# Kernel optimization log

Measured on AMD Instinct MI355X. Metric: run time of the kernel, lower is better.

Reference implementation:

```python
import jax, jax.numpy as jnp
import numpy as np

# (in_ch, out_ch) per conv layer per SA stage (use_xyz adds +3 to first in-ch)
DIMS = {1: [(3, 64), (64, 64), (64, 128)],
        2: [(131, 128), (128, 128), (128, 256)],
        3: [(259, 256), (256, 512), (512, 1024)]}
B, N = 32, 4096


def setup_inputs() -> dict:
    key = jax.random.key(0)
    key, k = jax.random.split(key)
    inp = {"pointcloud": jax.random.uniform(k, (B, N, 3), jnp.float32)}
    for s in (1, 2, 3):
        for l, (ci, co) in enumerate(DIMS[s]):
            key, k1, k2, k3 = jax.random.split(key, 4)
            inp[f"w{s}{l}"] = jax.random.normal(k1, (ci, co), jnp.float32) * (1.0 / np.sqrt(ci))
            # eval-mode BatchNorm folded to per-channel scale g and bias b
            inp[f"g{s}{l}"] = 1.0 + 0.1 * jax.random.normal(k2, (co,), jnp.float32)
            inp[f"b{s}{l}"] = 0.1 * jax.random.normal(k3, (co,), jnp.float32)
    return inp


def fps(xyz, npoint):
    """Farthest point sampling. xyz: (B,N,3) -> idx (B,npoint) int32. First index is 0."""
    n = xyz.shape[1]
    def one(pts):
        def body(carry, _):
            dist, last = carry
            d = jnp.sum((pts - pts[last]) ** 2, axis=-1)
            dist = jnp.minimum(dist, d)
            nxt = jnp.argmax(dist).astype(jnp.int32)
            return (dist, nxt), nxt
        init = (jnp.full((n,), 1e10, pts.dtype), jnp.int32(0))
        _, idxs = jax.lax.scan(body, init, None, length=npoint - 1)
        return jnp.concatenate([jnp.zeros((1,), jnp.int32), idxs])
    return jax.vmap(one)(xyz)


def ball_query(xyz, centers, radius, nsample):
    """xyz (B,N,3), centers (B,S,3) -> idx (B,S,nsample): first nsample in-ball point
    indices, deficits padded with the first found index (matches CUDA ball_query)."""
    n = xyz.shape[1]
    d2 = jnp.sum((centers[:, :, None, :] - xyz[:, None, :, :]) ** 2, axis=-1)  # (B,S,N)
    keyv = jnp.where(d2 < radius * radius, jnp.arange(n)[None, None, :], n)
    sk = jnp.sort(keyv, axis=-1)[..., :nsample]  # ascending valid indices, pad = n
    first = sk[..., :1]
    idx = jnp.where(sk == n, first, sk)
    return jnp.clip(idx, 0, n - 1)


def gather(pts, idx):
    """pts (B,N,C), idx (B,...) -> (B,...,C)"""
    return jax.vmap(lambda p, i: p[i])(pts, idx)


def shared_mlp(x, params):
    """x (..., Cin); each layer: 1x1 conv (matmul) + folded-BN affine + ReLU."""
    for w, g, b in params:
        x = jax.nn.relu(jnp.einsum('...c,cd->...d', x, w) * g + b)
    return x


def sa_module(xyz, feat, npoint, radius, nsample, params):
    ctr_idx = fps(xyz, npoint)
    new_xyz = gather(xyz, ctr_idx)                        # (B,S,3)
    idx = ball_query(xyz, new_xyz, radius, nsample)       # (B,S,K)
    g_xyz = gather(xyz, idx) - new_xyz[:, :, None, :]     # (B,S,K,3) centered
    grouped = g_xyz if feat is None else jnp.concatenate([g_xyz, gather(feat, idx)], axis=-1)
    h = shared_mlp(grouped, params)                       # (B,S,K,Cout)
    return new_xyz, jnp.max(h, axis=2)                    # max-pool over neighbors


def reference(pointcloud, w10, g10, b10, w11, g11, b11, w12, g12, b12,
              w20, g20, b20, w21, g21, b21, w22, g22, b22,
              w30, g30, b30, w31, g31, b31, w32, g32, b32):
    p1 = [(w10, g10, b10), (w11, g11, b11), (w12, g12, b12)]
    p2 = [(w20, g20, b20), (w21, g21, b21), (w22, g22, b22)]
    p3 = [(w30, g30, b30), (w31, g31, b31), (w32, g32, b32)]
    xyz = pointcloud[..., :3]
    xyz, feat = sa_module(xyz, None, 512, 0.2, 64, p1)
    xyz, feat = sa_module(xyz, feat, 128, 0.4, 64, p2)
    # group-all SA: one group containing all points, xyz NOT centered
    grouped = jnp.concatenate([xyz, feat], axis=-1)[:, None]  # (B,1,S,259)
    h = shared_mlp(grouped, p3)                                # (B,1,S,1024)
    return jnp.max(h, axis=2)[:, 0]                            # (B,1024)
```

## Files before the change

kernel.cpp:

```cpp
#include <hip/hip_runtime.h>
#include <math.h>

#define NTH 256

using short8 = __attribute__((ext_vector_type(8))) short;
using f32x4  = __attribute__((ext_vector_type(4))) float;

__device__ __forceinline__ unsigned short f2bf(float x) {
    unsigned u = __float_as_uint(x);
    u += 0x7fff + ((u >> 16) & 1);
    return (unsigned short)(u >> 16);
}
__device__ __forceinline__ float bf2f(unsigned short h) {
    return __uint_as_float(((unsigned)h) << 16);
}

template<int CTRL>
__device__ __forceinline__ unsigned long long dppmax(unsigned long long k) {
    unsigned lo = (unsigned)k, hi = (unsigned)(k >> 32);
    unsigned plo = (unsigned)__builtin_amdgcn_update_dpp(0, (int)lo, CTRL, 0xF, 0xF, true);
    unsigned phi = (unsigned)__builtin_amdgcn_update_dpp(0, (int)hi, CTRL, 0xF, 0xF, true);
    unsigned long long p = ((unsigned long long)phi << 32) | plo;
    return p > k ? p : k;
}

template<int N, int NPOINT, int NTHR, int NPC, bool INIT, bool SPILL>
__device__ __forceinline__ void fps_body(
    const float* __restrict__ xyz, float* __restrict__ out_xyz, int b, int it0,
    float* __restrict__ pts , float* __restrict__ ctr ,
    unsigned long long* __restrict__ wkey ,
    float* __restrict__ sdist, int* __restrict__ slast)
{
    constexpr int PT = N / NTHR;
    constexpr int NW = NTHR / 64;
    const int tid  = threadIdx.x;
    const int lane = tid & 63;
    const int w    = tid >> 6;
    const float* src = xyz + (size_t)b * N * 3;

    __builtin_amdgcn_s_setprio(1);

    for (int e = tid; e < N * 3; e += NTHR) pts[e] = src[e];

    float px[PT], py[PT], pz[PT], dist[PT];
    unsigned klo[PT];
#pragma unroll
    for (int j = 0; j < PT; ++j) {
        int i = j * NTHR + tid;
        px[j] = src[i * 3 + 0]; py[j] = src[i * 3 + 1]; pz[j] = src[i * 3 + 2];
        klo[j] = ~(unsigned)i;
        dist[j] = 1e10f;
    }
    int last = 0;
    if constexpr (!INIT) {
        const float* sd = sdist + (size_t)b * N;
#pragma unroll
        for (int j = 0; j < PT; ++j) dist[j] = sd[j * NTHR + tid];
        last = slast[b];
    } else {
        if (tid == 0) { ctr[0] = src[0]; ctr[1] = src[1]; ctr[2] = src[2]; }
    }
    __syncthreads();

    constexpr int CBEG = INIT ? 1 : 0;
    for (int c = CBEG; c < NPC; ++c) {
        const float lx = pts[last * 3 + 0];
        const float ly = pts[last * 3 + 1];
        const float lz = pts[last * 3 + 2];
        unsigned long long best = 0ull;
#pragma unroll
        for (int j = 0; j < PT; ++j) {
            float dx = px[j] - lx, dy = py[j] - ly, dz = pz[j] - lz;
            float d = __fadd_rn(__fadd_rn(__fmul_rn(dx, dx), __fmul_rn(dy, dy)),
                                __fmul_rn(dz, dz));
            float nd = fminf(dist[j], d);
            dist[j] = nd;
            unsigned long long key =
                ((unsigned long long)__float_as_uint(nd) << 32) | (unsigned long long)klo[j];
            best = (key > best) ? key : best;
        }
        best = dppmax<0xB1>(best);
        best = dppmax<0x4E>(best);
        best = dppmax<0x141>(best);
        best = dppmax<0x140>(best);
        best = dppmax<0x142>(best);
        best = dppmax<0x143>(best);
        const int p = (c & 1) * NW;
        if (lane == 63) wkey[p + w] = best;
        __syncthreads();
        unsigned long long K0[NW];
#pragma unroll
        for (int v = 0; v < NW; ++v) K0[v] = wkey[p + v];
#pragma unroll
        for (int st = NW / 2; st > 0; st >>= 1)
#pragma unroll
            for (int v = 0; v < st; ++v) K0[v] = (K0[v + st] > K0[v]) ? K0[v + st] : K0[v];
        last = (int)(~(unsigned)K0[0]);
        if (tid == 0) {
            ctr[c * 3 + 0] = pts[last * 3 + 0];
            ctr[c * 3 + 1] = pts[last * 3 + 1];
            ctr[c * 3 + 2] = pts[last * 3 + 2];
        }
    }
    __syncthreads();
    if constexpr (SPILL) {
        float* sd = sdist + (size_t)b * N;
#pragma unroll
        for (int j = 0; j < PT; ++j) sd[j * NTHR + tid] = dist[j];
        if (tid == 0) slast[b] = last;
    }
    float* dst = out_xyz + ((size_t)b * NPOINT + (it0 - CBEG)) * 3;
    for (int e = tid; e < NPC * 3; e += NTHR) dst[e] = ctr[e];
    __builtin_amdgcn_s_setprio(0);
}

template<int N, int NPOINT>
__device__ __forceinline__ void fps2_wave_body(
    const float* __restrict__ xyz, float* __restrict__ out_xyz, int b,
    float* __restrict__ pts , float* __restrict__ ctr )
{
    const int tid = threadIdx.x;
    const float* src = xyz + (size_t)b * N * 3;
    for (int e = tid; e < N * 3; e += NTH) pts[e] = src[e];
    __syncthreads();
    if (tid < 64) {
        __builtin_amdgcn_s_setprio(1);
        constexpr int PT = N / 64;
        const int lane = tid;
        float px[PT], py[PT], pz[PT], dist[PT];
        unsigned klo[PT];
#pragma unroll
        for (int j = 0; j < PT; ++j) {
            int i = j * 64 + lane;
            px[j] = pts[i * 3 + 0]; py[j] = pts[i * 3 + 1]; pz[j] = pts[i * 3 + 2];
            dist[j] = 1e10f;
            klo[j] = ~(unsigned)i;
        }
        int last = 0;
        if (lane == 0) { ctr[0] = pts[0]; ctr[1] = pts[1]; ctr[2] = pts[2]; }
        for (int it = 1; it < NPOINT; ++it) {
            const float lx = pts[last * 3 + 0];
            const float ly = pts[last * 3 + 1];
            const float lz = pts[last * 3 + 2];
            unsigned long long best = 0ull;
#pragma unroll
            for (int j = 0; j < PT; ++j) {
                float dx = px[j] - lx, dy = py[j] - ly, dz = pz[j] - lz;
                float d = __fadd_rn(__fadd_rn(__fmul_rn(dx, dx), __fmul_rn(dy, dy)),
                                    __fmul_rn(dz, dz));
                float nd = fminf(dist[j], d);
                dist[j] = nd;
                unsigned long long key =
                    ((unsigned long long)__float_as_uint(nd) << 32) | (unsigned long long)klo[j];
                best = (key > best) ? key : best;
            }
            best = dppmax<0xB1>(best);
            best = dppmax<0x4E>(best);
            best = dppmax<0x141>(best);
            best = dppmax<0x140>(best);
            best = dppmax<0x142>(best);
            best = dppmax<0x143>(best);
            unsigned long long g = __shfl(best, 63);
            last = (int)(~(unsigned)g);
            if (lane == 0) {
                ctr[it * 3 + 0] = pts[last * 3 + 0];
                ctr[it * 3 + 1] = pts[last * 3 + 1];
                ctr[it * 3 + 2] = pts[last * 3 + 2];
            }
        }
        __builtin_amdgcn_s_setprio(0);
    }
    __syncthreads();
    float* dst = out_xyz + (size_t)b * NPOINT * 3;
    for (int e = tid; e < NPOINT * 3; e += NTH) dst[e] = ctr[e];
}

#define PREP_TOT 813056
__device__ __forceinline__ void prep_body(
    int gid, int stride,
    const float* __restrict__ w0, const float* __restrict__ w1, const float* __restrict__ w2,
    const float* __restrict__ w3, const float* __restrict__ w4, const float* __restrict__ w5,
    const float* __restrict__ w6, const float* __restrict__ w7, const float* __restrict__ w8,
    unsigned short* __restrict__ outw)
{
    const int K_[9]    = {3, 64, 64, 131, 128, 128, 259, 256, 512};
    const int N_[9]    = {64, 64, 128, 128, 128, 256, 256, 512, 1024};
    const int E_[9]    = {2048, 4096, 8192, 20480, 16384, 32768, 73728, 131072, 524288};
    const int base_[9] = {0, 4096, 12288, 28672, 69632, 102400, 167936, 315392, 577536};
    const int PCF_[9]  = {0, 0, 0, 128, 0, 0, 256, 0, 0};
    const float* W_[9] = {w0, w1, w2, w3, w4, w5, w6, w7, w8};
    for (; gid < PREP_TOT; gid += stride) {
        int i = 0, t = gid;
        while (t >= E_[i]) { t -= E_[i]; ++i; }
        const int Nn = N_[i];
        const int k8 = t / (Nn * 8);
        const int rem = t - k8 * Nn * 8;
        const int col = rem >> 3, j = rem & 7;
        const int k = k8 * 8 + j;
        float v = 0.f;
        if (k < K_[i]) {
            int ks = k;
            const int pcf = PCF_[i];
            if (pcf > 0) ks = (k < pcf) ? (k + 3) : (k - pcf);
            v = W_[i][(size_t)ks * Nn + col];
        }
        unsigned short hi = f2bf(v);
        unsigned short lo = f2bf(v - bf2f(hi));
        outw[base_[i] + t] = hi;
        outw[base_[i] + E_[i] + t] = lo;
    }
}

template<int K, int NSUB, int NOFF, int NFULL, int RTILES, int SX, int SY, bool FINAL>
__device__ __forceinline__ void mfma_layer(
    const unsigned short* __restrict__ whi, const unsigned short* __restrict__ wlo,
    const float* __restrict__ gm, const float* __restrict__ bt,
    const unsigned short* __restrict__ Xhi, const unsigned short* __restrict__ Xlo,
    unsigned short* __restrict__ Yhi, unsigned short* __restrict__ Ylo,
    float* outp, int tid)
{
    constexpr int KP  = (K + 31) & ~31;
    constexpr int KC  = KP / 32;
    constexpr int NTW = NSUB / 64;
    static_assert(NSUB % 64 == 0, "col split");
    const int w = tid >> 6, lane = tid & 63;
    const int lr = lane & 15, lg = lane >> 4;
    const int colbase = NOFF + w * (NSUB / 4);

    f32x4 acc[RTILES][NTW];
#pragma unroll
    for (int m = 0; m < RTILES; ++m)
#pragma unroll
        for (int t = 0; t < NTW; ++t) acc[m][t] = f32x4{0.f, 0.f, 0.f, 0.f};

    const unsigned short* xh0 = Xhi + lr * SX + lg * 8;
    const unsigned short* xl0 = Xlo + lr * SX + lg * 8;

    for (int kc = 0; kc < KC; ++kc) {
        const size_t krow = (size_t)(kc * 4 + lg) * NFULL * 8;
        short8 bh[NTW], bl[NTW];
#pragma unroll
        for (int t = 0; t < NTW; ++t) {
            const int col = colbase + t * 16 + lr;
            bh[t] = *reinterpret_cast<const short8*>(whi + krow + (size_t)col * 8);
            bl[t] = *reinterpret_cast<const short8*>(wlo + krow + (size_t)col * 8);
        }
#pragma unroll
        for (int m = 0; m < RTILES; ++m) {
            short8 ah = *reinterpret_cast<const short8*>(xh0 + m * 16 * SX + kc * 32);
            short8 al = *reinterpret_cast<const short8*>(xl0 + m * 16 * SX + kc * 32);
#pragma unroll
            for (int t = 0; t < NTW; ++t) {
                acc[m][t] = __builtin_amdgcn_mfma_f32_16x16x32_bf16(ah, bh[t], acc[m][t], 0, 0, 0);
                acc[m][t] = __builtin_amdgcn_mfma_f32_16x16x32_bf16(ah, bl[t], acc[m][t], 0, 0, 0);
                acc[m][t] = __builtin_amdgcn_mfma_f32_16x16x32_bf16(al, bh[t], acc[m][t], 0, 0, 0);
            }
        }
    }
#pragma unroll
    for (int t = 0; t < NTW; ++t) {
        const int col = colbase + t * 16 + lr;
        const float gv = gm[col], bv = bt[col];
        if constexpr (FINAL) {
            float mx = 0.f;
#pragma unroll
            for (int m = 0; m < RTILES; ++m)
#pragma unroll
                for (int r = 0; r < 4; ++r)
                    mx = fmaxf(mx, fmaxf(fmaf(acc[m][t][r], gv, bv), 0.f));
            mx = fmaxf(mx, __shfl_xor(mx, 16));
            mx = fmaxf(mx, __shfl_xor(mx, 32));
            if (lg == 0)
                atomicMax(reinterpret_cast<int*>(outp) + col, __float_as_int(mx));
        } else {
#pragma unroll
            for (int m = 0; m < RTILES; ++m)
#pragma unroll
                for (int r = 0; r < 4; ++r) {
                    float v = fmaxf(fmaf(acc[m][t][r], gv, bv), 0.f);
                    unsigned short hi = f2bf(v);
                    unsigned short lo = f2bf(v - bf2f(hi));
                    const int row = m * 16 + lg * 4 + r;
                    Yhi[row * SY + col] = hi;
                    Ylo[row * SY + col] = lo;
                }
        }
    }
}

template<int CF, int C0, int C1, int C2, int R>
struct SaCfg {
    static constexpr int CIN = 3 + CF;
    static constexpr int KP0 = (CIN + 31) & ~31;
    static constexpr int SX = KP0 + 8, SY1 = C0 + 8, SY2 = C1 + 8;
    static constexpr int RT = R / 16;
    static constexpr int OFF_Y1 = 0;
    static constexpr int OFF_X = 2 * R * SY1;
    static constexpr int XSZ = 2 * R * SX, Y2SZ = 2 * R * SY2;
    static constexpr int TOT = OFF_X + (XSZ > Y2SZ ? XSZ : Y2SZ);
    static constexpr int BYTES = TOT * 2 + 264 * 4;
};

template<int CF, int C0, int C1, int C2, int R>
__device__ __forceinline__ void sa_body(
    unsigned short* __restrict__ sm, int* __restrict__ bqm,
    int b, int cs, int S, int half,
    const float* __restrict__ src_xyz, const float* __restrict__ src_feat,
    const float* __restrict__ centers,
    const unsigned short* __restrict__ w0h, const unsigned short* __restrict__ w0l,
    const unsigned short* __restrict__ w1h, const unsigned short* __restrict__ w1l,
    const unsigned short* __restrict__ w2h, const unsigned short* __restrict__ w2l,
    const float* __restrict__ g0, const float* __restrict__ b0,
    const float* __restrict__ g1, const float* __restrict__ b1,
    const float* __restrict__ g2, const float* __restrict__ b2,
    float* __restrict__ out_feat, int N, float r2)
{
    using C = SaCfg<CF, C0, C1, C2, R>;
    constexpr int TPR = NTH / R;
    const int tid  = threadIdx.x;
    const int lane = tid & 63;
    const int w    = tid >> 6;
    const int bs   = b * S + cs;

    const float cx = centers[(size_t)bs * 3 + 0];
    const float cy = centers[(size_t)bs * 3 + 1];
    const float cz = centers[(size_t)bs * 3 + 2];

    {
        const int seg = N >> 2;
        const float* px = src_xyz + (size_t)b * N * 3;
        int count = 0, first = -1;
        const int bend = (w + 1) * seg;
        for (int base = w * seg; base < bend && count < 64; base += 64) {
            int i = base + lane;
            float dx = px[i * 3 + 0] - cx, dy = px[i * 3 + 1] - cy, dz = px[i * 3 + 2] - cz;
            float d2 = __fadd_rn(__fadd_rn(__fmul_rn(dx, dx), __fmul_rn(dy, dy)),
                                 __fmul_rn(dz, dz));
            bool inb = d2 < r2;
            unsigned long long m = __ballot(inb);
            if (first < 0 && m) first = base + (__ffsll(m) - 1);
            if (inb) {
                int pos = count + (int)__popcll(m & ((1ull << lane) - 1ull));
                if (pos < 64) bqm[w * 64 + pos] = i;
            }
            count += (int)__popcll(m);
        }
        if (lane == 0) {
            bqm[256 + w] = count > 64 ? 64 : count;
            bqm[260 + w] = first;
        }
    }
    __syncthreads();

    unsigned short* Xhi = sm + C::OFF_X;    unsigned short* Xlo = Xhi + R * C::SX;
    unsigned short* Y1h = sm + C::OFF_Y1;   unsigned short* Y1l = Y1h + R * C::SY1;
    unsigned short* Y2h = sm + C::OFF_X;    unsigned short* Y2l = Y2h + R * C::SY2;

    {
        const int r = tid / TPR, s = tid % TPR;
        int pid;
        {
            const int cA = bqm[256 + 0], cB = bqm[256 + 1], cC = bqm[256 + 2], cD = bqm[256 + 3];
            const int tot = cA + cB + cC + cD;
            int t = half * R + r;
            if (t < tot) {
                int ww = 0;
                if (t >= cA) { t -= cA; ww = 1;
                    if (t >= cB) { t -= cB; ww = 2;
                        if (t >= cC) { t -= cC; ww = 3; } } }
                pid = bqm[ww * 64 + t];
            } else {
                const int fA = bqm[260 + 0], fB = bqm[260 + 1], fC = bqm[260 + 2], fD = bqm[260 + 3];
                pid = fA >= 0 ? fA : (fB >= 0 ? fB : (fC >= 0 ? fC : (fD >= 0 ? fD : (N - 1))));
            }
        }
        unsigned short* xh = Xhi + r * C::SX;
        unsigned short* xl = Xlo + r * C::SX;
        if constexpr (CF > 0) {
            constexpr int CPT = CF / TPR;
            const float* frow = src_feat + ((size_t)b * N + pid) * CF + s * CPT;
#pragma unroll
            for (int q = 0; q < CPT / 4; ++q) {
                float4 v4 = *reinterpret_cast<const float4*>(frow + q * 4);
                ushort4 h, l;
                h.x = f2bf(v4.x); l.x = f2bf(v4.x - bf2f(h.x));
                h.y = f2bf(v4.y); l.y = f2bf(v4.y - bf2f(h.y));
                h.z = f2bf(v4.z); l.z = f2bf(v4.z - bf2f(h.z));
                h.w = f2bf(v4.w); l.w = f2bf(v4.w - bf2f(h.w));
                *reinterpret_cast<ushort4*>(xh + s * CPT + q * 4) = h;
                *reinterpret_cast<ushort4*>(xl + s * CPT + q * 4) = l;
            }
        }
        if (s < 3) {
            float p = src_xyz[((size_t)b * N + pid) * 3 + s]
                      - (s == 0 ? cx : (s == 1 ? cy : cz));
            unsigned short hi = f2bf(p), lo = f2bf(p - bf2f(hi));
            xh[CF + s] = hi; xl[CF + s] = lo;
        }
        constexpr int PADPER = (C::KP0 - C::CIN + TPR - 1) / TPR;
#pragma unroll
        for (int q = 0; q < PADPER; ++q) {
            int c = C::CIN + s * PADPER + q;
            if (c < C::KP0) { xh[c] = 0; xl[c] = 0; }
        }
    }
    __syncthreads();
    mfma_layer<C::CIN, C0, 0, C0, C::RT, C::SX, C::SY1, false>(
        w0h, w0l, g0, b0, Xhi, Xlo, Y1h, Y1l, nullptr, tid);
    __syncthreads();
    mfma_layer<C0, C1, 0, C1, C::RT, C::SY1, C::SY2, false>(
        w1h, w1l, g1, b1, Y1h, Y1l, Y2h, Y2l, nullptr, tid);
    __syncthreads();
    mfma_layer<C1, C2, 0, C2, C::RT, C::SY2, 0, true>(
        w2h, w2l, g2, b2, Y2h, Y2l, nullptr, nullptr,
        out_feat + (size_t)bs * C2, tid);
}

template<int N1>
__global__ __launch_bounds__(NTH) void k_fps1a_prep(
    const float* __restrict__ pc, float* __restrict__ nxyz1,
    const float* __restrict__ w0, const float* __restrict__ w1, const float* __restrict__ w2,
    const float* __restrict__ w3, const float* __restrict__ w4, const float* __restrict__ w5,
    const float* __restrict__ w6, const float* __restrict__ w7, const float* __restrict__ w8,
    unsigned short* __restrict__ outw,
    float* __restrict__ sdist, int* __restrict__ slast,
    float4* __restrict__ z1, int n1, float4* __restrict__ z2, int n2,
    float4* __restrict__ z3, int n3, int nfps, int nprep)
{
    __shared__ float pts[N1 * 3];
    __shared__ float ctr[256 * 3];
    __shared__ unsigned long long wkey[2 * (NTH / 64)];
    if ((int)blockIdx.x < nfps) {
        fps_body<N1, 512, NTH, 256, true, true>(pc, nxyz1, blockIdx.x, 1,
                                                pts, ctr, wkey, sdist, slast);
    } else if ((int)blockIdx.x < nfps + nprep) {
        prep_body((blockIdx.x - nfps) * NTH + threadIdx.x, nprep * NTH,
                  w0, w1, w2, w3, w4, w5, w6, w7, w8, outw);
    } else {
        const int zid = (blockIdx.x - nfps - nprep) * NTH + threadIdx.x;
        const int zs  = (gridDim.x - nfps - nprep) * NTH;
        const float4 zv = make_float4(0.f, 0.f, 0.f, 0.f);
        for (int i = zid; i < n1; i += zs) z1[i] = zv;
        for (int i = zid; i < n2; i += zs) z2[i] = zv;
        for (int i = zid; i < n3; i += zs) z3[i] = zv;
    }
}

__global__ __launch_bounds__(NTH) void k_fps1b_sa1h1(
    const float* __restrict__ pc, float* __restrict__ nxyz1,
    float* __restrict__ sdist, int* __restrict__ slast,
    const unsigned short* __restrict__ w0h, const unsigned short* __restrict__ w0l,
    const unsigned short* __restrict__ w1h, const unsigned short* __restrict__ w1l,
    const unsigned short* __restrict__ w2h, const unsigned short* __restrict__ w2l,
    const float* __restrict__ g0, const float* __restrict__ b0,
    const float* __restrict__ g1, const float* __restrict__ b1,
    const float* __restrict__ g2, const float* __restrict__ b2,
    float* __restrict__ feat1, float r2)
{
    constexpr int FPSB = 4096 * 3 * 4 + 256 * 3 * 4 + 2 * (NTH / 64) * 8;
    constexpr int SAB  = SaCfg<0, 64, 64, 128, 64>::BYTES;
    constexpr int BYTES = FPSB > SAB ? FPSB : SAB;
    __shared__ __align__(16) char raw[BYTES];
    if ((int)blockIdx.x < 32) {
        float* pts = (float*)raw;
        float* ctr = (float*)(raw + 4096 * 3 * 4);
        unsigned long long* wkey = (unsigned long long*)(raw + 4096 * 3 * 4 + 256 * 3 * 4);
        fps_body<4096, 512, NTH, 256, false, false>(pc, nxyz1, blockIdx.x, 256,
                                                    pts, ctr, wkey, sdist, slast);
    } else {
        const int blk = blockIdx.x - 32;
        const int b = blk >> 8, cs = blk & 255;
        unsigned short* sm = (unsigned short*)raw;
        int* bqm = (int*)(raw + SaCfg<0, 64, 64, 128, 64>::TOT * 2);
        sa_body<0, 64, 64, 128, 64>(sm, bqm, b, cs, 512, 0,
                                    pc, nullptr, nxyz1,
                                    w0h, w0l, w1h, w1l, w2h, w2l,
                                    g0, b0, g1, b1, g2, b2, feat1, 4096, r2);
    }
}

__global__ __launch_bounds__(NTH) void k_fps2_sa1h2(
    const float* __restrict__ pc, const float* __restrict__ nxyz1,
    float* __restrict__ nxyz2,
    const unsigned short* __restrict__ w0h, const unsigned short* __restrict__ w0l,
    const unsigned short* __restrict__ w1h, const unsigned short* __restrict__ w1l,
    const unsigned short* __restrict__ w2h, const unsigned short* __restrict__ w2l,
    const float* __restrict__ g0, const float* __restrict__ b0,
    const float* __restrict__ g1, const float* __restrict__ b1,
    const float* __restrict__ g2, const float* __restrict__ b2,
    float* __restrict__ feat1, float r2)
{
    constexpr int FPSB = 512 * 3 * 4 + 128 * 3 * 4;
    constexpr int SAB  = SaCfg<0, 64, 64, 128, 64>::BYTES;
    constexpr int BYTES = FPSB > SAB ? FPSB : SAB;
    __shared__ __align__(16) char raw[BYTES];
    if ((int)blockIdx.x < 32) {
        float* pts = (float*)raw;
        float* ctr = (float*)(raw + 512 * 3 * 4);
        fps2_wave_body<512, 128>(nxyz1, nxyz2, blockIdx.x, pts, ctr);
    } else {
        const int blk = blockIdx.x - 32;
        const int b = blk >> 8, cs = 256 + (blk & 255);
        unsigned short* sm = (unsigned short*)raw;
        int* bqm = (int*)(raw + SaCfg<0, 64, 64, 128, 64>::TOT * 2);
        sa_body<0, 64, 64, 128, 64>(sm, bqm, b, cs, 512, 0,
                                    pc, nullptr, nxyz1,
                                    w0h, w0l, w1h, w1l, w2h, w2l,
                                    g0, b0, g1, b1, g2, b2, feat1, 4096, r2);
    }
}

__global__ __launch_bounds__(NTH) void k_sa2(
    const float* __restrict__ nxyz1, const float* __restrict__ feat1,
    const float* __restrict__ nxyz2,
    const unsigned short* __restrict__ w0h, const unsigned short* __restrict__ w0l,
    const unsigned short* __restrict__ w1h, const unsigned short* __restrict__ w1l,
    const unsigned short* __restrict__ w2h, const unsigned short* __restrict__ w2l,
    const float* __restrict__ g0, const float* __restrict__ b0,
    const float* __restrict__ g1, const float* __restrict__ b1,
    const float* __restrict__ g2, const float* __restrict__ b2,
    float* __restrict__ feat2, float r2)
{
    using C = SaCfg<128, 128, 128, 256, 32>;
    __shared__ __align__(16) char raw[C::BYTES];
    const int half = blockIdx.x & 1;
    const int cb   = blockIdx.x >> 1;
    const int b = cb >> 7, cs = cb & 127;
    unsigned short* sm = (unsigned short*)raw;
    int* bqm = (int*)(raw + C::TOT * 2);
    sa_body<128, 128, 128, 256, 32>(sm, bqm, b, cs, 128, half,
                                    nxyz1, feat1, nxyz2,
                                    w0h, w0l, w1h, w1l, w2h, w2l,
                                    g0, b0, g1, b1, g2, b2, feat2, 512, r2);
}

template<int CF, int C0, int C1, int C2>
__global__ __launch_bounds__(NTH) void head_mfma(
    const float* __restrict__ xyz, const float* __restrict__ feat,
    const unsigned short* __restrict__ w0h, const unsigned short* __restrict__ w0l,
    const unsigned short* __restrict__ w1h, const unsigned short* __restrict__ w1l,
    const unsigned short* __restrict__ w2h, const unsigned short* __restrict__ w2l,
    const float* __restrict__ g0, const float* __restrict__ b0,
    const float* __restrict__ g1, const float* __restrict__ b1,
    const float* __restrict__ g2, const float* __restrict__ b2,
    float* __restrict__ out, int Np)
{
    constexpr int R = 16;
    constexpr int CIN = 3 + CF;
    constexpr int KP0 = (CIN + 31) & ~31;
    constexpr int SX = KP0 + 8, SY1 = C0 + 8, SY2 = C1 + 8;
    constexpr int OFF_Y1 = 0;
    constexpr int OFF_X  = 2 * R * SY1;
    constexpr int XSZ = 2 * R * SX, Y2SZ = 2 * R * SY2;
    constexpr int TOT = OFF_X + (XSZ > Y2SZ ? XSZ : Y2SZ);
    __shared__ __align__(16) unsigned short sm[TOT];
    constexpr int TPR = NTH / R;

    const int tid = threadIdx.x;
    const int chunks = Np / R;
    const int b  = blockIdx.x / chunks;
    const int r0 = (blockIdx.x % chunks) * R;

    unsigned short* Xhi = sm + OFF_X;   unsigned short* Xlo = Xhi + R * SX;
    unsigned short* Y1h = sm + OFF_Y1;  unsigned short* Y1l = Y1h + R * SY1;
    unsigned short* Y2h = sm + OFF_X;   unsigned short* Y2l = Y2h + R * SY2;

    {
        const int r = tid / TPR, s = tid % TPR;
        const int row = r0 + r;
        unsigned short* xh = Xhi + r * SX;
        unsigned short* xl = Xlo + r * SX;
        constexpr int CPT = CF / TPR;
        const float* frow = feat + ((size_t)b * Np + row) * CF + s * CPT;
#pragma unroll
        for (int q = 0; q < CPT / 4; ++q) {
            float4 v4 = *reinterpret_cast<const float4*>(frow + q * 4);
            ushort4 h, l;
            h.x = f2bf(v4.x); l.x = f2bf(v4.x - bf2f(h.x));
            h.y = f2bf(v4.y); l.y = f2bf(v4.y - bf2f(h.y));
            h.z = f2bf(v4.z); l.z = f2bf(v4.z - bf2f(h.z));
            h.w = f2bf(v4.w); l.w = f2bf(v4.w - bf2f(h.w));
            *reinterpret_cast<ushort4*>(xh + s * CPT + q * 4) = h;
            *reinterpret_cast<ushort4*>(xl + s * CPT + q * 4) = l;
        }
        if (s < 3) {
            float p = xyz[((size_t)b * Np + row) * 3 + s];
            unsigned short hi = f2bf(p), lo = f2bf(p - bf2f(hi));
            xh[CF + s] = hi; xl[CF + s] = lo;
        }
        constexpr int PADPER = (KP0 - CIN + TPR - 1) / TPR;
#pragma unroll
        for (int q = 0; q < PADPER; ++q) {
            int c = CIN + s * PADPER + q;
            if (c < KP0) { xh[c] = 0; xl[c] = 0; }
        }
    }
    __syncthreads();
    mfma_layer<CIN, C0, 0, C0, 1, SX, SY1, false>(w0h, w0l, g0, b0, Xhi, Xlo, Y1h, Y1l, nullptr, tid);
    __syncthreads();
    mfma_layer<C0, C1, 0, C1, 1, SY1, SY2, false>(w1h, w1l, g1, b1, Y1h, Y1l, Y2h, Y2l, nullptr, tid);
    __syncthreads();
    float* op = out + (size_t)b * C2;
    mfma_layer<C1, C2 / 2, 0,      C2, 1, SY2, 0, true>(w2h, w2l, g2, b2, Y2h, Y2l, nullptr, nullptr, op, tid);
    mfma_layer<C1, C2 / 2, C2 / 2, C2, 1, SY2, 0, true>(w2h, w2l, g2, b2, Y2h, Y2l, nullptr, nullptr, op, tid);
}

extern "C" void kernel_launch(void* const* d_in, const int* in_sizes, int n_in,
                              void* d_out, int out_size, void* d_ws, size_t ws_size,
                              hipStream_t stream)
{
    (void)in_sizes; (void)n_in; (void)ws_size;
    const int B = 32;
    const float* pc = (const float*)d_in[0];
    const float* W[27];
    for (int i = 0; i < 27; ++i) W[i] = (const float*)d_in[1 + i];
    float* out = (float*)d_out;

    char* ws = (char*)d_ws;
    size_t off = 0;
    auto take = [&](size_t bytes) {
        void* p = ws + off;
        off += (bytes + 255) & ~(size_t)255;
        return p;
    };
    float* nxyz1 = (float*)take((size_t)B * 512 * 3 * 4);
    float* feat1 = (float*)take((size_t)B * 512 * 128 * 4);
    float* nxyz2 = (float*)take((size_t)B * 128 * 3 * 4);
    float* feat2 = (float*)take((size_t)B * 128 * 256 * 4);
    unsigned short* wf = (unsigned short*)take((size_t)1626112 * 2);
    float* sdist = (float*)take((size_t)B * 4096 * 4);
    int*   slast = (int*)take((size_t)B * 4);

    const int E_[9]    = {2048, 4096, 8192, 20480, 16384, 32768, 73728, 131072, 524288};
    const int base_[9] = {0, 4096, 12288, 28672, 69632, 102400, 167936, 315392, 577536};
    const unsigned short* wh[9]; const unsigned short* wl[9];
    for (int i = 0; i < 9; ++i) { wh[i] = wf + base_[i]; wl[i] = wf + base_[i] + E_[i]; }

    const float r2_1 = (float)(0.2 * 0.2);
    const float r2_2 = (float)(0.4 * 0.4);

    k_fps1a_prep<4096><<<32 + 512 + 64, NTH, 0, stream>>>(
        pc, nxyz1,
        W[0], W[3], W[6], W[9], W[12], W[15], W[18], W[21], W[24],
        wf, sdist, slast,
        (float4*)feat1, B * 512 * 128 / 4,
        (float4*)feat2, B * 128 * 256 / 4,
        (float4*)out,   out_size / 4,
        32, 512);

    k_fps1b_sa1h1<<<32 + B * 256, NTH, 0, stream>>>(
        pc, nxyz1, sdist, slast,
        wh[0], wl[0], wh[1], wl[1], wh[2], wl[2],
        W[1], W[2], W[4], W[5], W[7], W[8],
        feat1, r2_1);

    k_fps2_sa1h2<<<32 + B * 256, NTH, 0, stream>>>(
        pc, nxyz1, nxyz2,
        wh[0], wl[0], wh[1], wl[1], wh[2], wl[2],
        W[1], W[2], W[4], W[5], W[7], W[8],
        feat1, r2_1);

    k_sa2<<<B * 128 * 2, NTH, 0, stream>>>(
        nxyz1, feat1, nxyz2,
        wh[3], wl[3], wh[4], wl[4], wh[5], wl[5],
        W[10], W[11], W[13], W[14], W[16], W[17],
        feat2, r2_2);

    head_mfma<256, 256, 512, 1024><<<B * 8, NTH, 0, stream>>>(
        nxyz2, feat2,
        wh[6], wl[6], wh[7], wl[7], wh[8], wl[8],
        W[19], W[20], W[22], W[23], W[25], W[26],
        out, 128);
}
```

Measured before the change: 607.4 us.

## Merge FPS1b, FPS2 and SA1 into one kernel with per-chunk release/acquire flags

```diff
diff --git a/kernel.cpp b/kernel.cpp
--- a/kernel.cpp
+++ b/kernel.cpp
@@ -24,11 +24,11 @@
     return p > k ? p : k;
 }
 
-template<int N, int NPOINT, int NTHR, int NPC, bool INIT, bool SPILL>
-__device__ __forceinline__ void fps_body(
-    const float* __restrict__ xyz, float* __restrict__ out_xyz, int b, int it0,
-    float* __restrict__ pts , float* __restrict__ ctr ,
-    unsigned long long* __restrict__ wkey ,
+template<int N, int NPOINT, int NTHR, int NPC>
+__device__ __forceinline__ void fps1a_body(
+    const float* __restrict__ xyz, float* __restrict__ out_xyz, int b,
+    float* __restrict__ pts, float* __restrict__ ctr ,
+    unsigned long long* __restrict__ wkey,
     float* __restrict__ sdist, int* __restrict__ slast)
 {
     constexpr int PT = N / NTHR;
@@ -39,7 +39,6 @@
     const float* src = xyz + (size_t)b * N * 3;
 
     __builtin_amdgcn_s_setprio(1);
-
     for (int e = tid; e < N * 3; e += NTHR) pts[e] = src[e];
 
     float px[PT], py[PT], pz[PT], dist[PT];
@@ -52,18 +51,10 @@
         dist[j] = 1e10f;
     }
     int last = 0;
-    if constexpr (!INIT) {
-        const float* sd = sdist + (size_t)b * N;
-#pragma unroll
-        for (int j = 0; j < PT; ++j) dist[j] = sd[j * NTHR + tid];
-        last = slast[b];
-    } else {
-        if (tid == 0) { ctr[0] = src[0]; ctr[1] = src[1]; ctr[2] = src[2]; }
-    }
-    __syncthreads();
-
-    constexpr int CBEG = INIT ? 1 : 0;
-    for (int c = CBEG; c < NPC; ++c) {
+    if (tid == 0) { ctr[0] = src[0]; ctr[1] = src[1]; ctr[2] = src[2]; }
+    __syncthreads();
+
+    for (int c = 1; c < NPC; ++c) {
         const float lx = pts[last * 3 + 0];
         const float ly = pts[last * 3 + 1];
         const float lz = pts[last * 3 + 2];
@@ -103,21 +94,107 @@
         }
     }
     __syncthreads();
-    if constexpr (SPILL) {
+    {
         float* sd = sdist + (size_t)b * N;
 #pragma unroll
         for (int j = 0; j < PT; ++j) sd[j * NTHR + tid] = dist[j];
         if (tid == 0) slast[b] = last;
     }
-    float* dst = out_xyz + ((size_t)b * NPOINT + (it0 - CBEG)) * 3;
+    float* dst = out_xyz + (size_t)b * NPOINT * 3;
     for (int e = tid; e < NPC * 3; e += NTHR) dst[e] = ctr[e];
+    __builtin_amdgcn_s_setprio(0);
+}
+
+template<int N, int NTHR>
+__device__ __forceinline__ void fps1b_body(
+    const float* __restrict__ xyz, float* __restrict__ out_xyz , int b,
+    float* __restrict__ pts, float* __restrict__ ctr ,
+    unsigned long long* __restrict__ wkey,
+    const float* __restrict__ sdist, const int* __restrict__ slast,
+    int* __restrict__ flags)
+{
+    constexpr int PT = N / NTHR;
+    constexpr int NW = NTHR / 64;
+    const int tid  = threadIdx.x;
+    const int lane = tid & 63;
+    const int w    = tid >> 6;
+    const float* src = xyz + (size_t)b * N * 3;
+
+    __builtin_amdgcn_s_setprio(1);
+    for (int e = tid; e < N * 3; e += NTHR) pts[e] = src[e];
+
+    float px[PT], py[PT], pz[PT], dist[PT];
+    unsigned klo[PT];
+#pragma unroll
+    for (int j = 0; j < PT; ++j) {
+        int i = j * NTHR + tid;
+        px[j] = src[i * 3 + 0]; py[j] = src[i * 3 + 1]; pz[j] = src[i * 3 + 2];
+        klo[j] = ~(unsigned)i;
+    }
+    {
+        const float* sd = sdist + (size_t)b * N;
+#pragma unroll
+        for (int j = 0; j < PT; ++j) dist[j] = sd[j * NTHR + tid];
+    }
+    int last = slast[b];
+    __syncthreads();
+
+    for (int c = 0; c < 256; ++c) {
+        const float lx = pts[last * 3 + 0];
+        const float ly = pts[last * 3 + 1];
+        const float lz = pts[last * 3 + 2];
+        unsigned long long best = 0ull;
+#pragma unroll
+        for (int j = 0; j < PT; ++j) {
+            float dx = px[j] - lx, dy = py[j] - ly, dz = pz[j] - lz;
+            float d = __fadd_rn(__fadd_rn(__fmul_rn(dx, dx), __fmul_rn(dy, dy)),
+                                __fmul_rn(dz, dz));
+            float nd = fminf(dist[j], d);
+            dist[j] = nd;
+            unsigned long long key =
+                ((unsigned long long)__float_as_uint(nd) << 32) | (unsigned long long)klo[j];
+            best = (key > best) ? key : best;
+        }
+        best = dppmax<0xB1>(best);
+        best = dppmax<0x4E>(best);
+        best = dppmax<0x141>(best);
+        best = dppmax<0x140>(best);
+        best = dppmax<0x142>(best);
+        best = dppmax<0x143>(best);
+        const int p = (c & 1) * NW;
+        if (lane == 63) wkey[p + w] = best;
+        __syncthreads();
+        unsigned long long K0[NW];
+#pragma unroll
+        for (int v = 0; v < NW; ++v) K0[v] = wkey[p + v];
+#pragma unroll
+        for (int st = NW / 2; st > 0; st >>= 1)
+#pragma unroll
+            for (int v = 0; v < st; ++v) K0[v] = (K0[v + st] > K0[v]) ? K0[v + st] : K0[v];
+        last = (int)(~(unsigned)K0[0]);
+        if (tid == 0) {
+            ctr[c * 3 + 0] = pts[last * 3 + 0];
+            ctr[c * 3 + 1] = pts[last * 3 + 1];
+            ctr[c * 3 + 2] = pts[last * 3 + 2];
+        }
+        if ((c & 63) == 63) {
+            const int q = c >> 6;
+            __syncthreads();
+            float* dst = out_xyz + ((size_t)b * 512 + 256 + q * 64) * 3;
+            for (int e = tid; e < 192; e += NTHR) dst[e] = ctr[q * 192 + e];
+            __syncthreads();
+            if (tid == 0)
+                __hip_atomic_store(&flags[b * 4 + q], 1,
+                                   __ATOMIC_RELEASE, __HIP_MEMORY_SCOPE_AGENT);
+        }
+    }
     __builtin_amdgcn_s_setprio(0);
 }
 
 template<int N, int NPOINT>
 __device__ __forceinline__ void fps2_wave_body(
     const float* __restrict__ xyz, float* __restrict__ out_xyz, int b,
-    float* __restrict__ pts , float* __restrict__ ctr )
+    float* __restrict__ pts, float* __restrict__ ctr)
 {
     const int tid = threadIdx.x;
     const float* src = xyz + (size_t)b * N * 3;
@@ -425,14 +502,14 @@
     unsigned short* __restrict__ outw,
     float* __restrict__ sdist, int* __restrict__ slast,
     float4* __restrict__ z1, int n1, float4* __restrict__ z2, int n2,
-    float4* __restrict__ z3, int n3, int nfps, int nprep)
+    float4* __restrict__ z3, int n3, float4* __restrict__ z4, int n4,
+    int nfps, int nprep)
 {
     __shared__ float pts[N1 * 3];
     __shared__ float ctr[256 * 3];
     __shared__ unsigned long long wkey[2 * (NTH / 64)];
     if ((int)blockIdx.x < nfps) {
-        fps_body<N1, 512, NTH, 256, true, true>(pc, nxyz1, blockIdx.x, 1,
-                                                pts, ctr, wkey, sdist, slast);
+        fps1a_body<N1, 512, NTH, 256>(pc, nxyz1, blockIdx.x, pts, ctr, wkey, sdist, slast);
     } else if ((int)blockIdx.x < nfps + nprep) {
         prep_body((blockIdx.x - nfps) * NTH + threadIdx.x, nprep * NTH,
                   w0, w1, w2, w3, w4, w5, w6, w7, w8, outw);
@@ -440,15 +517,17 @@
         const int zid = (blockIdx.x - nfps - nprep) * NTH + threadIdx.x;
         const int zs  = (gridDim.x - nfps - nprep) * NTH;
         const float4 zv = make_float4(0.f, 0.f, 0.f, 0.f);
+        for (int i = zid; i < n4; i += zs) z4[i] = zv;
         for (int i = zid; i < n1; i += zs) z1[i] = zv;
         for (int i = zid; i < n2; i += zs) z2[i] = zv;
         for (int i = zid; i < n3; i += zs) z3[i] = zv;
     }
 }
 
-__global__ __launch_bounds__(NTH) void k_fps1b_sa1h1(
-    const float* __restrict__ pc, float* __restrict__ nxyz1,
-    float* __restrict__ sdist, int* __restrict__ slast,
+__global__ __launch_bounds__(NTH) void k_fps1b2_sa1(
+    const float* __restrict__ pc, float* __restrict__ nxyz1, float* __restrict__ nxyz2,
+    const float* __restrict__ sdist, const int* __restrict__ slast,
+    int* __restrict__ flags,
     const unsigned short* __restrict__ w0h, const unsigned short* __restrict__ w0l,
     const unsigned short* __restrict__ w1h, const unsigned short* __restrict__ w1l,
     const unsigned short* __restrict__ w2h, const unsigned short* __restrict__ w2l,
@@ -462,45 +541,33 @@
     constexpr int BYTES = FPSB > SAB ? FPSB : SAB;
     __shared__ __align__(16) char raw[BYTES];
     if ((int)blockIdx.x < 32) {
-        float* pts = (float*)raw;
-        float* ctr = (float*)(raw + 4096 * 3 * 4);
-        unsigned long long* wkey = (unsigned long long*)(raw + 4096 * 3 * 4 + 256 * 3 * 4);
-        fps_body<4096, 512, NTH, 256, false, false>(pc, nxyz1, blockIdx.x, 256,
-                                                    pts, ctr, wkey, sdist, slast);
+        const int b = blockIdx.x;
+        {
+            float* pts = (float*)raw;
+            float* ctr = (float*)(raw + 4096 * 3 * 4);
+            unsigned long long* wkey = (unsigned long long*)(raw + 4096 * 3 * 4 + 256 * 3 * 4);
+            fps1b_body<4096, NTH>(pc, nxyz1, b, pts, ctr, wkey, sdist, slast, flags);
+        }
+        __syncthreads();
+        {
+            float* pts = (float*)raw;
+            float* ctr = (float*)(raw + 512 * 3 * 4);
+            fps2_wave_body<512, 128>(nxyz1, nxyz2, b, pts, ctr);
+        }
     } else {
         const int blk = blockIdx.x - 32;
-        const int b = blk >> 8, cs = blk & 255;
-        unsigned short* sm = (unsigned short*)raw;
-        int* bqm = (int*)(raw + SaCfg<0, 64, 64, 128, 64>::TOT * 2);
-        sa_body<0, 64, 64, 128, 64>(sm, bqm, b, cs, 512, 0,
-                                    pc, nullptr, nxyz1,
-                                    w0h, w0l, w1h, w1l, w2h, w2l,
-                                    g0, b0, g1, b1, g2, b2, feat1, 4096, r2);
-    }
-}
-
-__global__ __launch_bounds__(NTH) void k_fps2_sa1h2(
-    const float* __restrict__ pc, const float* __restrict__ nxyz1,
-    float* __restrict__ nxyz2,
-    const unsigned short* __restrict__ w0h, const unsigned short* __restrict__ w0l,
-    const unsigned short* __restrict__ w1h, const unsigned short* __restrict__ w1l,
-    const unsigned short* __restrict__ w2h, const unsigned short* __restrict__ w2l,
-    const float* __restrict__ g0, const float* __restrict__ b0,
-    const float* __restrict__ g1, const float* __restrict__ b1,
-    const float* __restrict__ g2, const float* __restrict__ b2,
-    float* __restrict__ feat1, float r2)
-{
-    constexpr int FPSB = 512 * 3 * 4 + 128 * 3 * 4;
-    constexpr int SAB  = SaCfg<0, 64, 64, 128, 64>::BYTES;
-    constexpr int BYTES = FPSB > SAB ? FPSB : SAB;
-    __shared__ __align__(16) char raw[BYTES];
-    if ((int)blockIdx.x < 32) {
-        float* pts = (float*)raw;
-        float* ctr = (float*)(raw + 512 * 3 * 4);
-        fps2_wave_body<512, 128>(nxyz1, nxyz2, blockIdx.x, pts, ctr);
-    } else {
-        const int blk = blockIdx.x - 32;
-        const int b = blk >> 8, cs = 256 + (blk & 255);
+        const int g = blk / (32 * 64);
+        const int o = blk % (32 * 64);
+        const int b = o >> 6;
+        const int cs = g * 64 + (o & 63);
+        if (cs >= 256) {
+            if (threadIdx.x == 0) {
+                while (__hip_atomic_load(&flags[b * 4 + ((cs >> 6) - 4)],
+                                         __ATOMIC_ACQUIRE, __HIP_MEMORY_SCOPE_AGENT) == 0)
+                    __builtin_amdgcn_s_sleep(8);
+            }
+            __syncthreads();
+        }
         unsigned short* sm = (unsigned short*)raw;
         int* bqm = (int*)(raw + SaCfg<0, 64, 64, 128, 64>::TOT * 2);
         sa_body<0, 64, 64, 128, 64>(sm, bqm, b, cs, 512, 0,
@@ -630,6 +697,7 @@
     unsigned short* wf = (unsigned short*)take((size_t)1626112 * 2);
     float* sdist = (float*)take((size_t)B * 4096 * 4);
     int*   slast = (int*)take((size_t)B * 4);
+    int*   flags = (int*)take((size_t)B * 4 * 4);
 
     const int E_[9]    = {2048, 4096, 8192, 20480, 16384, 32768, 73728, 131072, 524288};
     const int base_[9] = {0, 4096, 12288, 28672, 69632, 102400, 167936, 315392, 577536};
@@ -646,16 +714,11 @@
         (float4*)feat1, B * 512 * 128 / 4,
         (float4*)feat2, B * 128 * 256 / 4,
         (float4*)out,   out_size / 4,
+        (float4*)flags, B * 4 * 4 / 16,
         32, 512);
 
-    k_fps1b_sa1h1<<<32 + B * 256, NTH, 0, stream>>>(
-        pc, nxyz1, sdist, slast,
-        wh[0], wl[0], wh[1], wl[1], wh[2], wl[2],
-        W[1], W[2], W[4], W[5], W[7], W[8],
-        feat1, r2_1);
-
-    k_fps2_sa1h2<<<32 + B * 256, NTH, 0, stream>>>(
-        pc, nxyz1, nxyz2,
+    k_fps1b2_sa1<<<32 + B * 512, NTH, 0, stream>>>(
+        pc, nxyz1, nxyz2, sdist, slast, flags,
         wh[0], wl[0], wh[1], wl[1], wh[2], wl[2],
         W[1], W[2], W[4], W[5], W[7], W[8],
         feat1, r2_1);
```

Result: no change. 598.4 us (-1.5%).
